# Optimization experiments

Hardware: AMD Instinct MI355X
Metric: run time of the kernel (lower is better)

The kernel has to match this reference:

```python
import jax, jax.numpy as jnp
import numpy as np

B, T, C = 2, 2048, 1024
E = 8            # num_experts
K = 2            # num_active (top-k)
H = 4 * C        # expert hidden dim


def setup_inputs() -> dict:
    key = jax.random.key(0)
    ks = jax.random.split(key, 8)
    s = 0.02
    return {
        "x": jax.random.normal(ks[0], (B, T, C), dtype=jnp.float32),
        "Wg": jax.random.normal(ks[1], (C, E), dtype=jnp.float32) * s,
        "bg": jnp.zeros((E,), dtype=jnp.float32),
        "W1": jax.random.normal(ks[2], (E, C, H), dtype=jnp.float32) * s,
        "b1": jnp.zeros((E, H), dtype=jnp.float32),
        "W2": jax.random.normal(ks[3], (E, H, C), dtype=jnp.float32) * s,
        "b2": jnp.zeros((E, C), dtype=jnp.float32),
    }


def reference(x, Wg, bg, W1, b1, W2, b2):
    Bs, Ts, Cs = x.shape
    x_flat = x.reshape(-1, Cs)                       # [N, C]
    gate_logits = x_flat @ Wg + bg                   # [N, E]
    gates = jax.nn.softmax(gate_logits, axis=-1)
    w, idx = jax.lax.top_k(gates, K)                 # [N, K]
    w = w / jnp.sum(w, axis=-1, keepdims=True)
    # combine[n, e] = sum_k w[n,k] * (idx[n,k] == e); zero for unrouted experts,
    # so weighting the dense per-expert output reproduces the masked scatter-add.
    combine = jnp.sum(jax.nn.one_hot(idx, E, dtype=x.dtype) * w[..., None], axis=1)  # [N, E]
    out = jnp.zeros_like(x_flat)
    for e in range(E):  # small fixed expert loop; GEMM-dominated
        h = jax.nn.gelu(x_flat @ W1[e] + b1[e], approximate=False)  # [N, H]
        y = h @ W2[e] + b2[e]                                       # [N, C]
        out = out + y * combine[:, e:e + 1]
    return out.reshape(Bs, Ts, Cs)
```

## Files before the change

kernel.cpp:

```cpp
#include <hip/hip_runtime.h>
#include <hip/hip_bf16.h>
#include <math.h>

#define NTOK  4096
#define CDIM  1024
#define HDIM  4096
#define NEXP  8
#define TOPK  2

using short8 = __attribute__((ext_vector_type(8))) short;
using f32x4  = __attribute__((ext_vector_type(4))) float;

__device__ inline ushort f2bf(float f) {
    uint32_t u = __builtin_bit_cast(uint32_t, f);
    uint32_t r = (u + 0x7FFFu + ((u >> 16) & 1u)) >> 16;
    return (ushort)r;
}

__device__ __forceinline__ float gelu_fast(float v) {
    float z = fabsf(v) * 0.70710678118654752f;
    float t = 1.0f / fmaf(0.3275911f, z, 1.0f);
    float p = t * fmaf(t, fmaf(t, fmaf(t, fmaf(t, 1.061405429f, -1.453152027f),
                                        1.421413741f), -0.284496736f), 0.254829592f);
    float erfz = 1.0f - p * __expf(-z * z);
    return 0.5f * v * (1.0f + copysignf(erfz, v));
}

__device__ __forceinline__ void gl_lds16(const void* g, void* l) {
    __builtin_amdgcn_global_load_lds(
        (const __attribute__((address_space(1))) void*)(void*)g,
        (__attribute__((address_space(3))) void*)l, 16, 0, 0);
}

#define SCHED_FENCE() __builtin_amdgcn_sched_barrier(0)
#define RAW_BAR()  { SCHED_FENCE(); __builtin_amdgcn_s_barrier(); SCHED_FENCE(); }

__global__ __launch_bounds__(256)
void gate_kernel(const float* __restrict__ x, const float* __restrict__ Wg,
                 const float* __restrict__ bg, int* __restrict__ counts,
                 int* __restrict__ tlist, float* __restrict__ wslot,
                 ushort* __restrict__ xbf) {
    int wave = threadIdx.x >> 6, lane = threadIdx.x & 63;
    int t = blockIdx.x * 4 + wave;
    const float* xr = x + (size_t)t * CDIM;

    float acc[NEXP];
#pragma unroll
    for (int e = 0; e < NEXP; e++) acc[e] = 0.f;

#pragma unroll
    for (int i = 0; i < CDIM / 64; i++) {
        int c = lane + 64 * i;
        float xv = xr[c];
        xbf[(size_t)t * CDIM + c] = f2bf(xv);
        const float* wr = Wg + (size_t)c * NEXP;
#pragma unroll
        for (int e = 0; e < NEXP; e++) acc[e] += xv * wr[e];
    }
#pragma unroll
    for (int e = 0; e < NEXP; e++) {
        float v = acc[e];
        for (int off = 32; off > 0; off >>= 1) v += __shfl_xor(v, off);
        acc[e] = v + bg[e];
    }
    if (lane == 0) {
        int i1 = 0; float m1 = acc[0];
#pragma unroll
        for (int e = 1; e < NEXP; e++) if (acc[e] > m1) { m1 = acc[e]; i1 = e; }
        int i2 = -1; float m2 = -1e30f;
#pragma unroll
        for (int e = 0; e < NEXP; e++) if (e != i1 && acc[e] > m2) { m2 = acc[e]; i2 = e; }
        float w0 = 1.f / (1.f + expf(m2 - m1));
        float w1 = 1.f - w0;
        int p0 = atomicAdd(&counts[i1], 1);
        tlist[i1 * NTOK + p0] = t * 2;
        int p1 = atomicAdd(&counts[i2], 1);
        tlist[i2 * NTOK + p1] = t * 2 + 1;
        wslot[t * 2]     = w0;
        wslot[t * 2 + 1] = w1;
    }
}

__global__ __launch_bounds__(256)
void transpose_kernel(const float* __restrict__ in, ushort* __restrict__ out,
                      int R, int Ccols) {
    __shared__ ushort tile[64 * 64];
    int e = blockIdx.z;
    const float* src = in + (size_t)e * R * Ccols;
    ushort* dst = out + (size_t)e * Ccols * R;
    int c0 = blockIdx.x * 64, r0 = blockIdx.y * 64;
    int tid = threadIdx.x;
    int tx = tid & 15, ty = tid >> 4;

    float4 v[4];
#pragma unroll
    for (int j = 0; j < 4; j++)
        v[j] = *(const float4*)&src[(size_t)(r0 + ty * 4 + j) * Ccols + c0 + tx * 4];

#pragma unroll
    for (int i = 0; i < 4; i++) {
        int c = tx * 4 + i;
        uint2 pr;
        pr.x = (uint)f2bf(v[0][i]) | ((uint)f2bf(v[1][i]) << 16);
        pr.y = (uint)f2bf(v[2][i]) | ((uint)f2bf(v[3][i]) << 16);
        int gr = (ty >> 1) ^ ((c >> 2) & 7);
        int off = c * 128 + (gr << 4) + (ty & 1) * 8;
        *(uint2*)((char*)tile + off) = pr;
    }
    __syncthreads();

#pragma unroll
    for (int p = 0; p < 2; p++) {
        int c   = (tid >> 3) + 32 * p;
        int rch = tid & 7;
        int gr  = rch ^ ((c >> 2) & 7);
        short8 val = *(short8*)((char*)tile + c * 128 + (gr << 4));
        *(short8*)&dst[(size_t)(c0 + c) * R + r0 + rch * 8] = val;
    }
}

template<int GELU, int OUTBF16>
__global__ __launch_bounds__(256, 3)
void moe_gemm(const ushort* __restrict__ A, const ushort* __restrict__ Bt,
              const float* __restrict__ bias, const int* __restrict__ tlist,
              const int* __restrict__ counts, void* __restrict__ Out,
              int K, int N, int ashift, int nxmask, int nxshift, int ksplit,
              size_t psz) {
    int flat = blockIdx.x;
    int e  = flat & 7;
    int j  = flat >> 3;
    int mt = j & 31;
    int nj = j >> 5;
    int cnt = counts[e];
    int m0 = mt * 128;
    if (m0 >= cnt) return;
    int n0 = (nj & nxmask) * 128;
    int split = nj >> nxshift;
    int kbeg = split * ksplit;

    __shared__ ushort As[2][128 * 32];
    __shared__ ushort Bs[2][128 * 32];
    __shared__ int rowv[128];

    int tid = threadIdx.x;
    if (tid < 128) {
        int r = m0 + tid;
        rowv[tid] = tlist[e * NTOK + (r < cnt ? r : cnt - 1)];
    }
    __syncthreads();

    const ushort* Be = Bt + (size_t)e * N * K;

    int lane = tid & 63, w = tid >> 6;
    int wm = (w >> 1) * 64, wn = (w & 1) * 64;
    int quad = lane >> 4, l16 = lane & 15;

    int srow   = tid >> 2;
    int schunk = (tid & 3) ^ ((tid >> 3) & 3);
    const ushort* pa0 = A  + (size_t)(rowv[srow]      >> ashift) * K + kbeg + schunk * 8;
    const ushort* pa1 = A  + (size_t)(rowv[srow + 64] >> ashift) * K + kbeg + schunk * 8;
    const ushort* pb0 = Be + (size_t)(n0 + srow)      * K + kbeg + schunk * 8;
    const ushort* pb1 = Be + (size_t)(n0 + srow + 64) * K + kbeg + schunk * 8;

    int swr  = quad ^ ((l16 >> 1) & 3);
    int aidx = (wm + l16) * 32 + swr * 8;
    int bidx = (wn + l16) * 32 + swr * 8;

    f32x4 acc[4][4] = {};

    auto STAGE = [&](int buf) {
        gl_lds16(pa0, &As[buf][(w * 16) * 32]);
        gl_lds16(pa1, &As[buf][(w * 16 + 64) * 32]);
        gl_lds16(pb0, &Bs[buf][(w * 16) * 32]);
        gl_lds16(pb1, &Bs[buf][(w * 16 + 64) * 32]);
        pa0 += 32; pa1 += 32; pb0 += 32; pb1 += 32;
    };
    auto COMPUTE = [&](int buf) {
        short8 a[4], b[4];
#pragma unroll
        for (int mti = 0; mti < 4; mti++) a[mti] = *(short8*)&As[buf][aidx + mti * 512];
#pragma unroll
        for (int nti = 0; nti < 4; nti++) b[nti] = *(short8*)&Bs[buf][bidx + nti * 512];
#pragma unroll
        for (int mti = 0; mti < 4; mti++)
#pragma unroll
            for (int nti = 0; nti < 4; nti++)
                acc[mti][nti] = __builtin_amdgcn_mfma_f32_16x16x32_bf16(
                    a[mti], b[nti], acc[mti][nti], 0, 0, 0);
    };

    int nsteps = ksplit >> 5;
    STAGE(0);
    for (int i = 0; i < nsteps - 1; ++i) {
        int b = i & 1;
        STAGE(1 - b);
        asm volatile("s_waitcnt vmcnt(4)" ::: "memory");
        RAW_BAR();
        COMPUTE(b);
        RAW_BAR();
    }
    asm volatile("s_waitcnt vmcnt(0)" ::: "memory");
    RAW_BAR();
    COMPUTE((nsteps - 1) & 1);

    float* outF = (float*)Out + split * psz;
    ushort* outH = (ushort*)Out;
    const float* be = bias + (size_t)e * N;
    float bv[4];
#pragma unroll
    for (int nti = 0; nti < 4; nti++)
        bv[nti] = (split == 0) ? be[n0 + wn + nti * 16 + l16] : 0.f;
#pragma unroll
    for (int mti = 0; mti < 4; mti++) {
#pragma unroll
        for (int r = 0; r < 4; r++) {
            int lrow = wm + mti * 16 + quad * 4 + r;
            if (m0 + lrow < cnt) {
                int v = rowv[lrow];
                size_t base = (size_t)v * N;
#pragma unroll
                for (int nti = 0; nti < 4; nti++) {
                    int col = n0 + wn + nti * 16 + l16;
                    float val = acc[mti][nti][r] + bv[nti];
                    if (GELU) val = gelu_fast(val);
                    if (OUTBF16) outH[base + col] = f2bf(val);
                    else         outF[base + col] = val;
                }
            }
        }
    }
}

__global__ __launch_bounds__(256)
void combine_kernel(const float* __restrict__ y, const float* __restrict__ wslot,
                    float* __restrict__ out) {
    const float* y2 = y + (size_t)NTOK * TOPK * CDIM;
    int idx = blockIdx.x * 256 + threadIdx.x;
    int c4 = idx & (CDIM / 4 - 1);
    int t = idx >> 8;
    float w0 = wslot[2 * t], w1 = wslot[2 * t + 1];
    const float4* y0a = (const float4*)(y  + (size_t)(2 * t) * CDIM);
    const float4* y1a = (const float4*)(y  + (size_t)(2 * t + 1) * CDIM);
    const float4* y0b = (const float4*)(y2 + (size_t)(2 * t) * CDIM);
    const float4* y1b = (const float4*)(y2 + (size_t)(2 * t + 1) * CDIM);
    float4 a0 = y0a[c4], a1 = y0b[c4], b0 = y1a[c4], b1 = y1b[c4], o;
    o.x = w0 * (a0.x + a1.x) + w1 * (b0.x + b1.x);
    o.y = w0 * (a0.y + a1.y) + w1 * (b0.y + b1.y);
    o.z = w0 * (a0.z + a1.z) + w1 * (b0.z + b1.z);
    o.w = w0 * (a0.w + a1.w) + w1 * (b0.w + b1.w);
    ((float4*)(out + (size_t)t * CDIM))[c4] = o;
}

extern "C" void kernel_launch(void* const* d_in, const int* in_sizes, int n_in,
                              void* d_out, int out_size, void* d_ws, size_t ws_size,
                              hipStream_t stream) {
    const float* x  = (const float*)d_in[0];
    const float* Wg = (const float*)d_in[1];
    const float* bg = (const float*)d_in[2];
    const float* W1 = (const float*)d_in[3];
    const float* b1 = (const float*)d_in[4];
    const float* W2 = (const float*)d_in[5];
    const float* b2 = (const float*)d_in[6];
    float* out = (float*)d_out;
    char* ws = (char*)d_ws;

    size_t off = 0;
    int*    counts = (int*)(ws + off);    off += 256;
    int*    tlist  = (int*)(ws + off);    off += (size_t)NEXP * NTOK * 4;
    float*  wslot  = (float*)(ws + off);  off += (size_t)NTOK * TOPK * 4;
    ushort* xbf    = (ushort*)(ws + off); off += (size_t)NTOK * CDIM * 2;
    ushort* WT     = (ushort*)(ws + off); off += (size_t)NEXP * CDIM * HDIM * 2;
    ushort* h      = (ushort*)(ws + off); off += (size_t)NTOK * TOPK * HDIM * 2;
    float*  y      = (float*)(ws + off);  off += (size_t)NTOK * TOPK * CDIM * 4 * 2;

    hipMemsetAsync(counts, 0, NEXP * sizeof(int), stream);

    gate_kernel<<<NTOK / 4, 256, 0, stream>>>(x, Wg, bg, counts, tlist, wslot, xbf);

    transpose_kernel<<<dim3(HDIM / 64, CDIM / 64, NEXP), 256, 0, stream>>>(
        W1, WT, CDIM, HDIM);

    moe_gemm<1, 1><<<NEXP * 32 * (HDIM / 128), 256, 0, stream>>>(
        xbf, WT, b1, tlist, counts, (void*)h, CDIM, HDIM, 1,
        HDIM / 128 - 1, 5, CDIM, 0);

    transpose_kernel<<<dim3(CDIM / 64, HDIM / 64, NEXP), 256, 0, stream>>>(
        W2, WT, HDIM, CDIM);

    moe_gemm<0, 0><<<NEXP * 32 * (CDIM / 128) * 2, 256, 0, stream>>>(
        h, WT, b2, tlist, counts, (void*)y, HDIM, CDIM, 0,
        CDIM / 128 - 1, 3, HDIM / 2, (size_t)NTOK * TOPK * CDIM);

    combine_kernel<<<(NTOK * CDIM / 4) / 256, 256, 0, stream>>>(y, wslot, out);
}
```

Before: 656.8 us.

## Fuse fp32 weight transpose and bf16 conversion into MoE GEMM B-operand staging

Removes the two standalone transpose kernels that turned W1 and W2 into bf16 transposed copies before each GEMM. The GEMM now reads fp32 weight rows directly into registers, converts them to bf16 and writes them swizzled into LDS, pipelined over two register stages alongside the async A loads. This avoids a full read and write pass over both weight tensors and two launches. In exchange, each GEMM block re-reads fp32 weights at twice the byte size of bf16 across m-tiles, relying on cache reuse. It also adds conversion ALU work and register pressure inside the main loop.

```diff
diff --git a/kernel.cpp b/kernel.cpp
--- a/kernel.cpp
+++ b/kernel.cpp
@@ -34,6 +34,8 @@
 
 #define SCHED_FENCE() __builtin_amdgcn_sched_barrier(0)
 #define RAW_BAR()  { SCHED_FENCE(); __builtin_amdgcn_s_barrier(); SCHED_FENCE(); }
+#define VMWAIT(N)  { asm volatile("s_waitcnt vmcnt(" #N ")" ::: "memory"); SCHED_FENCE(); }
+#define LGKM0()    { asm volatile("s_waitcnt lgkmcnt(0)" ::: "memory"); SCHED_FENCE(); }
 
 __global__ __launch_bounds__(256)
 void gate_kernel(const float* __restrict__ x, const float* __restrict__ Wg,
@@ -81,47 +83,9 @@
     }
 }
 
-__global__ __launch_bounds__(256)
-void transpose_kernel(const float* __restrict__ in, ushort* __restrict__ out,
-                      int R, int Ccols) {
-    __shared__ ushort tile[64 * 64];
-    int e = blockIdx.z;
-    const float* src = in + (size_t)e * R * Ccols;
-    ushort* dst = out + (size_t)e * Ccols * R;
-    int c0 = blockIdx.x * 64, r0 = blockIdx.y * 64;
-    int tid = threadIdx.x;
-    int tx = tid & 15, ty = tid >> 4;
-
-    float4 v[4];
-#pragma unroll
-    for (int j = 0; j < 4; j++)
-        v[j] = *(const float4*)&src[(size_t)(r0 + ty * 4 + j) * Ccols + c0 + tx * 4];
-
-#pragma unroll
-    for (int i = 0; i < 4; i++) {
-        int c = tx * 4 + i;
-        uint2 pr;
-        pr.x = (uint)f2bf(v[0][i]) | ((uint)f2bf(v[1][i]) << 16);
-        pr.y = (uint)f2bf(v[2][i]) | ((uint)f2bf(v[3][i]) << 16);
-        int gr = (ty >> 1) ^ ((c >> 2) & 7);
-        int off = c * 128 + (gr << 4) + (ty & 1) * 8;
-        *(uint2*)((char*)tile + off) = pr;
-    }
-    __syncthreads();
-
-#pragma unroll
-    for (int p = 0; p < 2; p++) {
-        int c   = (tid >> 3) + 32 * p;
-        int rch = tid & 7;
-        int gr  = rch ^ ((c >> 2) & 7);
-        short8 val = *(short8*)((char*)tile + c * 128 + (gr << 4));
-        *(short8*)&dst[(size_t)(c0 + c) * R + r0 + rch * 8] = val;
-    }
-}
-
 template<int GELU, int OUTBF16>
 __global__ __launch_bounds__(256, 3)
-void moe_gemm(const ushort* __restrict__ A, const ushort* __restrict__ Bt,
+void moe_gemm(const ushort* __restrict__ A, const float* __restrict__ W,
               const float* __restrict__ bias, const int* __restrict__ tlist,
               const int* __restrict__ counts, void* __restrict__ Out,
               int K, int N, int ashift, int nxmask, int nxshift, int ksplit,
@@ -149,7 +113,7 @@
     }
     __syncthreads();
 
-    const ushort* Be = Bt + (size_t)e * N * K;
+    const float* We = W + (size_t)e * K * N;
 
     int lane = tid & 63, w = tid >> 6;
     int wm = (w >> 1) * 64, wn = (w & 1) * 64;
@@ -157,23 +121,46 @@
 
     int srow   = tid >> 2;
     int schunk = (tid & 3) ^ ((tid >> 3) & 3);
-    const ushort* pa0 = A  + (size_t)(rowv[srow]      >> ashift) * K + kbeg + schunk * 8;
-    const ushort* pa1 = A  + (size_t)(rowv[srow + 64] >> ashift) * K + kbeg + schunk * 8;
-    const ushort* pb0 = Be + (size_t)(n0 + srow)      * K + kbeg + schunk * 8;
-    const ushort* pb1 = Be + (size_t)(n0 + srow + 64) * K + kbeg + schunk * 8;
+    const ushort* pa0 = A + (size_t)(rowv[srow]      >> ashift) * K + kbeg + schunk * 8;
+    const ushort* pa1 = A + (size_t)(rowv[srow + 64] >> ashift) * K + kbeg + schunk * 8;
+
+    int q = tid >> 5, g = tid & 31;
+    const float* pB = We + (size_t)(kbeg + 4 * q) * N + n0 + 4 * g;
+    int boff[4];
+#pragma unroll
+    for (int i = 0; i < 4; i++) {
+        int n = 4 * g + i;
+        boff[i] = n * 64 + ((((q >> 1) ^ ((n >> 1) & 3))) << 4) + (q & 1) * 8;
+    }
 
     int swr  = quad ^ ((l16 >> 1) & 3);
     int aidx = (wm + l16) * 32 + swr * 8;
     int bidx = (wn + l16) * 32 + swr * 8;
 
     f32x4 acc[4][4] = {};
-
-    auto STAGE = [&](int buf) {
+    f32x4 r0a, r0b, r0c, r0d, r1a, r1b, r1c, r1d;
+
+#define BLOAD(s) { \
+        s##a = *(const f32x4*)(pB + 0 * (size_t)N); \
+        s##b = *(const f32x4*)(pB + 1 * (size_t)N); \
+        s##c = *(const f32x4*)(pB + 2 * (size_t)N); \
+        s##d = *(const f32x4*)(pB + 3 * (size_t)N); \
+        pB += 32 * (size_t)N; }
+
+#define DSW(s, buf) { \
+        char* bb = (char*)&Bs[buf][0]; \
+        _Pragma("unroll") \
+        for (int i = 0; i < 4; i++) { \
+            uint2 pr; \
+            pr.x = (uint)f2bf(s##a[i]) | ((uint)f2bf(s##b[i]) << 16); \
+            pr.y = (uint)f2bf(s##c[i]) | ((uint)f2bf(s##d[i]) << 16); \
+            *(uint2*)(bb + boff[i]) = pr; \
+        } }
+
+    auto AGLDS = [&](int buf) {
         gl_lds16(pa0, &As[buf][(w * 16) * 32]);
         gl_lds16(pa1, &As[buf][(w * 16 + 64) * 32]);
-        gl_lds16(pb0, &Bs[buf][(w * 16) * 32]);
-        gl_lds16(pb1, &Bs[buf][(w * 16 + 64) * 32]);
-        pa0 += 32; pa1 += 32; pb0 += 32; pb1 += 32;
+        pa0 += 32; pa1 += 32;
     };
     auto COMPUTE = [&](int buf) {
         short8 a[4], b[4];
@@ -190,18 +177,33 @@
     };
 
     int nsteps = ksplit >> 5;
-    STAGE(0);
-    for (int i = 0; i < nsteps - 1; ++i) {
-        int b = i & 1;
-        STAGE(1 - b);
-        asm volatile("s_waitcnt vmcnt(4)" ::: "memory");
-        RAW_BAR();
-        COMPUTE(b);
-        RAW_BAR();
-    }
-    asm volatile("s_waitcnt vmcnt(0)" ::: "memory");
+    BLOAD(r0); AGLDS(0);
+    for (int i = 0; i < nsteps - 2; i += 2) {
+        BLOAD(r1); AGLDS(1);
+        VMWAIT(6);
+        DSW(r0, 0); LGKM0();
+        RAW_BAR();
+        COMPUTE(0);
+        RAW_BAR();
+        BLOAD(r0); AGLDS(0);
+        VMWAIT(6);
+        DSW(r1, 1); LGKM0();
+        RAW_BAR();
+        COMPUTE(1);
+        RAW_BAR();
+    }
+    BLOAD(r1); AGLDS(1);
+    VMWAIT(6);
+    DSW(r0, 0); LGKM0();
     RAW_BAR();
-    COMPUTE((nsteps - 1) & 1);
+    COMPUTE(0);
+    RAW_BAR();
+    VMWAIT(0);
+    DSW(r1, 1); LGKM0();
+    RAW_BAR();
+    COMPUTE(1);
+#undef BLOAD
+#undef DSW
 
     float* outF = (float*)Out + split * psz;
     ushort* outH = (ushort*)Out;
@@ -269,7 +271,6 @@
     int*    tlist  = (int*)(ws + off);    off += (size_t)NEXP * NTOK * 4;
     float*  wslot  = (float*)(ws + off);  off += (size_t)NTOK * TOPK * 4;
     ushort* xbf    = (ushort*)(ws + off); off += (size_t)NTOK * CDIM * 2;
-    ushort* WT     = (ushort*)(ws + off); off += (size_t)NEXP * CDIM * HDIM * 2;
     ushort* h      = (ushort*)(ws + off); off += (size_t)NTOK * TOPK * HDIM * 2;
     float*  y      = (float*)(ws + off);  off += (size_t)NTOK * TOPK * CDIM * 4 * 2;
 
@@ -277,18 +278,12 @@
 
     gate_kernel<<<NTOK / 4, 256, 0, stream>>>(x, Wg, bg, counts, tlist, wslot, xbf);
 
-    transpose_kernel<<<dim3(HDIM / 64, CDIM / 64, NEXP), 256, 0, stream>>>(
-        W1, WT, CDIM, HDIM);
-
     moe_gemm<1, 1><<<NEXP * 32 * (HDIM / 128), 256, 0, stream>>>(
-        xbf, WT, b1, tlist, counts, (void*)h, CDIM, HDIM, 1,
+        xbf, W1, b1, tlist, counts, (void*)h, CDIM, HDIM, 1,
         HDIM / 128 - 1, 5, CDIM, 0);
 
-    transpose_kernel<<<dim3(CDIM / 64, HDIM / 64, NEXP), 256, 0, stream>>>(
-        W2, WT, HDIM, CDIM);
-
     moe_gemm<0, 0><<<NEXP * 32 * (CDIM / 128) * 2, 256, 0, stream>>>(
-        h, WT, b2, tlist, counts, (void*)y, HDIM, CDIM, 0,
+        h, W2, b2, tlist, counts, (void*)y, HDIM, CDIM, 0,
         CDIM / 128 - 1, 3, HDIM / 2, (size_t)NTOK * TOPK * CDIM);
 
     combine_kernel<<<(NTOK * CDIM / 4) / 256, 256, 0, stream>>>(y, wslot, out);
```

After: 742.2 us. +13.0%, slower.
